# Kernel tuning notes

Hardware: AMD Instinct MI355X
Metric: run time of the kernel (lower is better)

The kernel has to match this reference:

```python
import jax, jax.numpy as jnp
import numpy as np

B, L, D_MODEL = 2, 2048, 1024
D_STATE, D_CONV, EXPAND = 8, 4, 2
D_INNER = EXPAND * D_MODEL          # 2048
DT_RANK = (D_MODEL + 15) // 16      # 64


def setup_inputs() -> dict:
    key = jax.random.key(0)
    ks = jax.random.split(key, 8)
    s = 0.02
    x = jax.random.normal(ks[0], (B, L, D_MODEL), dtype=jnp.float32)
    W_in = jax.random.normal(ks[1], (D_MODEL, 2 * D_INNER), dtype=jnp.float32) * s
    dw_kernel = jax.random.normal(ks[2], (D_CONV, D_INNER), dtype=jnp.float32) * s  # depthwise
    pw_kernel = jax.random.normal(ks[3], (D_INNER, D_INNER), dtype=jnp.float32) * s  # pointwise
    conv_bias = jnp.zeros((D_INNER,), dtype=jnp.float32)
    W_x = jax.random.normal(ks[4], (D_INNER, DT_RANK + 2 * D_STATE), dtype=jnp.float32) * s
    W_dt = jax.random.normal(ks[5], (DT_RANK, D_INNER), dtype=jnp.float32) * s
    b_dt = jnp.zeros((D_INNER,), dtype=jnp.float32)
    # A = repeat(range(1..d_state), d_inner).reshape(d_inner, d_state), stored as log
    A_init = np.repeat(np.arange(1, D_STATE + 1, dtype=np.float32), D_INNER).reshape(D_INNER, D_STATE)
    A_log = jnp.asarray(np.log(A_init))
    D = jnp.ones((D_INNER,), dtype=jnp.float32)
    W_out = jax.random.normal(ks[6], (D_INNER, D_MODEL), dtype=jnp.float32) * s
    return {"x": x, "W_in": W_in, "dw_kernel": dw_kernel, "pw_kernel": pw_kernel,
            "conv_bias": conv_bias, "W_x": W_x, "W_dt": W_dt, "b_dt": b_dt,
            "A_log": A_log, "D": D, "W_out": W_out}


def reference(x, W_in, dw_kernel, pw_kernel, conv_bias, W_x, W_dt, b_dt, A_log, D, W_out):
    d_inner, d_state = A_log.shape
    dt_rank = W_dt.shape[0]
    d_conv = dw_kernel.shape[0]
    bsz = x.shape[0]

    xz = x @ W_in                                   # [B,L,2*di]
    x_in, z = jnp.split(xz, 2, axis=-1)             # each [B,L,di]

    # causal separable conv: depthwise (causal pad) -> pointwise -> swish
    xp = jnp.pad(x_in, ((0, 0), (d_conv - 1, 0), (0, 0)))
    xc = jax.lax.conv_general_dilated(
        xp, dw_kernel[:, None, :], window_strides=(1,), padding='VALID',
        dimension_numbers=('NWC', 'WIO', 'NWC'), feature_group_count=d_inner)
    xc = jax.nn.silu(xc @ pw_kernel + conv_bias)    # [B,L,di]

    x_dbl = xc @ W_x                                # [B,L,dt_rank+2*ds]
    delta = x_dbl[..., :dt_rank]
    Bm = x_dbl[..., dt_rank:dt_rank + d_state]      # [B,L,ds]
    C = x_dbl[..., dt_rank + d_state:]              # [B,L,ds]
    delta = jax.nn.softplus(delta @ W_dt + b_dt)    # [B,L,di]

    A = -jnp.exp(A_log)                             # [di,ds]
    deltaA = jnp.exp(jnp.einsum('bld,dn->bldn', delta, A))       # [B,L,di,ds]
    deltaB_u = jnp.einsum('bld,bln,bld->bldn', delta, Bm, xc)    # [B,L,di,ds]

    def step(h, inp):
        dA_t, dBu_t, C_t = inp
        h = dA_t * h + dBu_t                        # [B,di,ds]
        y_t = jnp.einsum('bn,bdn->bd', C_t, h)      # [B,di]
        return h, y_t

    h0 = jnp.zeros((bsz, d_inner, d_state), dtype=x.dtype)
    elems = (deltaA.transpose(1, 0, 2, 3), deltaB_u.transpose(1, 0, 2, 3), C.transpose(1, 0, 2))
    _, ys = jax.lax.scan(step, h0, elems)           # ys: [L,B,di]
    y = ys.transpose(1, 0, 2)                       # [B,L,di]

    y = y + xc * D
    y = y * jax.nn.silu(z)
    return y @ W_out                                # [B,L,d_model]
```

## Files before the change

kernel.cpp:

```cpp
#include <hip/hip_runtime.h>
#include <math.h>

#define Bb 2
#define Ll 2048
#define DMODEL 1024
#define DINNER 2048
#define DSTATE 8
#define DTRANK 64
#define DCONV 4
#define MM (Bb*Ll)
#define NCH 64
#define CL 32
#define G3_KCH 8
#define G3_KC (DINNER / G3_KCH)

typedef __attribute__((ext_vector_type(8))) short    bf16x8;
typedef __attribute__((ext_vector_type(4))) float    f32x4;

__device__ __forceinline__ float silu_f(float x) {
    return x / (1.0f + __expf(-x));
}
__device__ __forceinline__ float softplus_f(float x) {
    return fmaxf(x, 0.0f) + log1pf(__expf(-fabsf(x)));
}
__device__ __forceinline__ unsigned short f2bf(float f) {
    unsigned int u = __float_as_uint(f);
    u += 0x7fffu + ((u >> 16) & 1u);
    return (unsigned short)(u >> 16);
}
__device__ __forceinline__ void async_cp16(const unsigned short* g, unsigned short* l) {
    __builtin_amdgcn_global_load_lds(
        (const __attribute__((address_space(1))) void*)g,
        (__attribute__((address_space(3))) void*)l, 16, 0, 0);
}

template <int EPI>
__global__ __launch_bounds__(256) void mfma_gemm(
    const unsigned short* __restrict__ A, const unsigned short* __restrict__ Bt,
    float* __restrict__ C, int M, int N, int K,
    int lda, int ldb, int ldc, const float* __restrict__ bias)
{
    __shared__ unsigned short As[128 * 32];
    __shared__ unsigned short Bs[128 * 32];

    const int bm = blockIdx.y * 128;
    const int bn = blockIdx.x * 128;
    const int tid  = threadIdx.x;
    const int w    = tid >> 6;
    const int lane = tid & 63;
    const int wm = (w >> 1) * 64;
    const int wn = (w & 1) * 64;
    const int lr = lane & 15;
    const int lq = lane >> 4;

    const int r1 = w * 32 + (lane >> 2);
    const int sp = lane & 3;
    const int slog = sp ^ ((r1 >> 1) & 3);
    const unsigned short* gA1 = A  + (size_t)(bm + r1) * lda + slog * 8;
    const unsigned short* gA2 = gA1 + (size_t)16 * lda;
    const unsigned short* gB1 = Bt + (size_t)(bn + r1) * ldb + slog * 8;
    const unsigned short* gB2 = gB1 + (size_t)16 * ldb;
    unsigned short* lA1 = As + w * 1024;
    unsigned short* lA2 = As + w * 1024 + 512;
    unsigned short* lB1 = Bs + w * 1024;
    unsigned short* lB2 = Bs + w * 1024 + 512;

    const int fsw = (lq ^ ((lr >> 1) & 3)) * 8;

    f32x4 acc[4][4];
#pragma unroll
    for (int i = 0; i < 4; ++i)
#pragma unroll
        for (int j = 0; j < 4; ++j) acc[i][j] = (f32x4){0.f, 0.f, 0.f, 0.f};

    for (int k0 = 0; k0 < K; k0 += 32) {
        __syncthreads();
        async_cp16(gA1 + k0, lA1);
        async_cp16(gA2 + k0, lA2);
        async_cp16(gB1 + k0, lB1);
        async_cp16(gB2 + k0, lB2);
        __syncthreads();

        bf16x8 a[4], b[4];
#pragma unroll
        for (int i = 0; i < 4; ++i)
            a[i] = *(const bf16x8*)&As[(wm + i * 16 + lr) * 32 + fsw];
#pragma unroll
        for (int j = 0; j < 4; ++j)
            b[j] = *(const bf16x8*)&Bs[(wn + j * 16 + lr) * 32 + fsw];
#pragma unroll
        for (int i = 0; i < 4; ++i)
#pragma unroll
            for (int j = 0; j < 4; ++j)
                acc[i][j] = __builtin_amdgcn_mfma_f32_16x16x32_bf16(
                    a[i], b[j], acc[i][j], 0, 0, 0);
    }

#pragma unroll
    for (int i = 0; i < 4; ++i) {
        const int row0 = bm + wm + i * 16 + lq * 4;
#pragma unroll
        for (int j = 0; j < 4; ++j) {
            const int col = bn + wn + j * 16 + lr;
            float bv = (EPI == 1) ? bias[col] : 0.0f;
#pragma unroll
            for (int r = 0; r < 4; ++r) {
                float v = acc[i][j][r];
                if (EPI == 1) v = silu_f(v + bv);
                C[(size_t)(row0 + r) * ldc + col] = v;
            }
        }
    }
}

__global__ __launch_bounds__(256) void gemm_tiled_sp(
    const float* __restrict__ A, const float* __restrict__ B,
    float* __restrict__ C, int M, int N, int K,
    int lda, int ldb, int ldc, const float* __restrict__ bias)
{
    __shared__ float As[16][68];
    __shared__ float Bs[16][68];

    const int bm = blockIdx.y * 64;
    const int bn = blockIdx.x * 64;
    const int tid = threadIdx.x;
    const int tx = tid & 15;
    const int ty = tid >> 4;

    float acc[4][4];
#pragma unroll
    for (int i = 0; i < 4; ++i)
#pragma unroll
        for (int j = 0; j < 4; ++j) acc[i][j] = 0.0f;

    const int ar = tid >> 2;
    const int ac = (tid & 3) << 2;
    const int br = tid >> 4;
    const int bc = (tid & 15) << 2;

    for (int k0 = 0; k0 < K; k0 += 16) {
        float4 av = *(const float4*)&A[(size_t)(bm + ar) * lda + k0 + ac];
        float4 bv = *(const float4*)&B[(size_t)(k0 + br) * ldb + bn + bc];
        As[ac + 0][ar] = av.x;
        As[ac + 1][ar] = av.y;
        As[ac + 2][ar] = av.z;
        As[ac + 3][ar] = av.w;
        *(float4*)&Bs[br][bc] = bv;
        __syncthreads();
#pragma unroll
        for (int k = 0; k < 16; ++k) {
            float4 a4 = *(float4*)&As[k][ty * 4];
            float4 b4 = *(float4*)&Bs[k][tx * 4];
            float am[4] = {a4.x, a4.y, a4.z, a4.w};
            float bn4[4] = {b4.x, b4.y, b4.z, b4.w};
#pragma unroll
            for (int i = 0; i < 4; ++i)
#pragma unroll
                for (int j = 0; j < 4; ++j)
                    acc[i][j] = fmaf(am[i], bn4[j], acc[i][j]);
        }
        __syncthreads();
    }

    const int col = bn + tx * 4;
#pragma unroll
    for (int i = 0; i < 4; ++i) {
        int row = bm + ty * 4 + i;
        float4 v = make_float4(acc[i][0], acc[i][1], acc[i][2], acc[i][3]);
        v.x = softplus_f(v.x + bias[col + 0]);
        v.y = softplus_f(v.y + bias[col + 1]);
        v.z = softplus_f(v.z + bias[col + 2]);
        v.w = softplus_f(v.w + bias[col + 3]);
        *(float4*)&C[(size_t)row * ldc + col] = v;
    }
}

__global__ __launch_bounds__(256) void g3_splitk(
    const float* __restrict__ xc, const float* __restrict__ Wx,
    float* __restrict__ part)
{
    __shared__ float As[16][68];
    __shared__ float Bs[16][85];
    const int m0 = blockIdx.x * 64;
    const int kb = blockIdx.y * G3_KC;
    const int t = threadIdx.x;
    const int tr = t >> 4;
    const int tc = t & 15;

    const int arow = t >> 2;
    const int ak4  = (t & 3) * 4;
    const int bk   = t >> 4;
    const int bc   = (t & 15) * 5;

    float acc[4][5];
#pragma unroll
    for (int r = 0; r < 4; ++r)
#pragma unroll
        for (int c = 0; c < 5; ++c) acc[r][c] = 0.0f;

    for (int k0 = 0; k0 < G3_KC; k0 += 16) {
        float4 av = *(const float4*)&xc[(size_t)(m0 + arow) * DINNER + kb + k0 + ak4];
        float bv[5];
#pragma unroll
        for (int q = 0; q < 5; ++q)
            bv[q] = Wx[(size_t)(kb + k0 + bk) * 80 + bc + q];
        __syncthreads();
        As[ak4 + 0][arow] = av.x;
        As[ak4 + 1][arow] = av.y;
        As[ak4 + 2][arow] = av.z;
        As[ak4 + 3][arow] = av.w;
#pragma unroll
        for (int q = 0; q < 5; ++q) Bs[bk][bc + q] = bv[q];
        __syncthreads();
#pragma unroll
        for (int k = 0; k < 16; ++k) {
            float a[4], b[5];
#pragma unroll
            for (int r = 0; r < 4; ++r) a[r] = As[k][tr * 4 + r];
#pragma unroll
            for (int c = 0; c < 5; ++c) b[c] = Bs[k][tc * 5 + c];
#pragma unroll
            for (int r = 0; r < 4; ++r)
#pragma unroll
                for (int c = 0; c < 5; ++c)
                    acc[r][c] = fmaf(a[r], b[c], acc[r][c]);
        }
    }
#pragma unroll
    for (int r = 0; r < 4; ++r)
#pragma unroll
        for (int c = 0; c < 5; ++c)
            part[((size_t)blockIdx.y * MM + m0 + tr * 4 + r) * 80 + tc * 5 + c] = acc[r][c];
}

__global__ __launch_bounds__(256) void g3_reduce(
    const float* __restrict__ part, float* __restrict__ xdbl)
{
    int i = (blockIdx.x * 256 + threadIdx.x) * 4;
    if (i >= MM * 80) return;
    float4 s = *(const float4*)&part[i];
#pragma unroll
    for (int c = 1; c < G3_KCH; ++c) {
        float4 p = *(const float4*)&part[(size_t)c * MM * 80 + i];
        s.x += p.x; s.y += p.y; s.z += p.z; s.w += p.w;
    }
    *(float4*)&xdbl[i] = s;
}

__global__ __launch_bounds__(256) void transpose_cast(
    const float* __restrict__ src, unsigned short* __restrict__ dst, int R, int C)
{
    __shared__ float tile[32][33];
    const int c0 = blockIdx.x * 32;
    const int r0 = blockIdx.y * 32;
    const int tx = threadIdx.x;
    const int ty = threadIdx.y;
#pragma unroll
    for (int i = 0; i < 32; i += 8)
        tile[ty + i][tx] = src[(size_t)(r0 + ty + i) * C + c0 + tx];
    __syncthreads();
#pragma unroll
    for (int i = 0; i < 32; i += 8)
        dst[(size_t)(c0 + ty + i) * R + r0 + tx] = f2bf(tile[tx][ty + i]);
}

__global__ __launch_bounds__(256) void cast_bf16(
    const float* __restrict__ src, unsigned short* __restrict__ dst, int n)
{
    int i = (blockIdx.x * 256 + threadIdx.x) * 4;
    if (i >= n) return;
    float4 v = *(const float4*)&src[i];
    ushort4 o;
    o.x = f2bf(v.x); o.y = f2bf(v.y); o.z = f2bf(v.z); o.w = f2bf(v.w);
    *(ushort4*)&dst[i] = o;
}

__global__ __launch_bounds__(256) void dwconv_kernel(
    const float* __restrict__ x_in, const float* __restrict__ dwk,
    unsigned short* __restrict__ out)
{
    size_t i = (size_t)blockIdx.x * 256 + threadIdx.x;
    if (i >= (size_t)MM * DINNER) return;
    int d = (int)(i & (DINNER - 1));
    size_t bl = i >> 11;
    int l = (int)(bl & (Ll - 1));
    int b = (int)(bl >> 11);
    float acc = 0.0f;
#pragma unroll
    for (int k = 0; k < DCONV; ++k) {
        int t = l + k - (DCONV - 1);
        if (t >= 0)
            acc = fmaf(x_in[((size_t)(b * Ll + t)) * DINNER + d],
                       dwk[k * DINNER + d], acc);
    }
    out[i] = f2bf(acc);
}

__global__ __launch_bounds__(256) void scan_pass1(
    const float* __restrict__ delta, const float* __restrict__ xc,
    const float* __restrict__ xdbl, const float* __restrict__ A_log,
    float* __restrict__ cs_a, float* __restrict__ cs_h)
{
    const int d = blockIdx.x * 256 + threadIdx.x;
    const int c = blockIdx.y;
    const int b = blockIdx.z;
    const int t0 = c * CL;

    __shared__ float sB[CL][8];
    {
        int i = threadIdx.x;
        int t = i >> 3, j = i & 7;
        sB[t][j] = xdbl[((size_t)(b * Ll + t0 + t)) * 80 + DTRANK + j];
    }
    __syncthreads();

    float An[8];
#pragma unroll
    for (int n = 0; n < 8; ++n) An[n] = -__expf(A_log[d * 8 + n]);

    float h[8], ap[8];
#pragma unroll
    for (int n = 0; n < 8; ++n) { h[n] = 0.0f; ap[n] = 1.0f; }

    const float* dptr = delta + ((size_t)(b * Ll + t0)) * DINNER + d;
    const float* xptr = xc + ((size_t)(b * Ll + t0)) * DINNER + d;

#pragma unroll 4
    for (int t = 0; t < CL; ++t) {
        float dl = dptr[(size_t)t * DINNER];
        float xv = xptr[(size_t)t * DINNER];
        float du = dl * xv;
#pragma unroll
        for (int n = 0; n < 8; ++n) {
            float dA = __expf(dl * An[n]);
            h[n] = fmaf(dA, h[n], du * sB[t][n]);
            ap[n] *= dA;
        }
    }

    size_t base = (((size_t)(b * NCH + c)) * 8) * DINNER + d;
#pragma unroll
    for (int n = 0; n < 8; ++n) {
        cs_a[base + (size_t)n * DINNER] = ap[n];
        cs_h[base + (size_t)n * DINNER] = h[n];
    }
}

__global__ __launch_bounds__(256) void scan_pass2(
    const float* __restrict__ cs_a, const float* cs_h, float* hin)
{
    int idx = blockIdx.x * 256 + threadIdx.x;
    if (idx >= Bb * 8 * DINNER) return;
    int d = idx & (DINNER - 1);
    int n = (idx >> 11) & 7;
    int b = idx >> 14;
    float H = 0.0f;
    for (int c = 0; c < NCH; ++c) {
        size_t o = (((size_t)(b * NCH + c)) * 8 + n) * DINNER + d;
        float a = cs_a[o];
        float hh = cs_h[o];
        hin[o] = H;
        H = fmaf(a, H, hh);
    }
}

__global__ __launch_bounds__(256) void scan_pass3(
    const float* __restrict__ delta, const float* __restrict__ xc,
    const float* __restrict__ xdbl, const float* __restrict__ A_log,
    const float* __restrict__ hin, const float* __restrict__ z,
    const float* __restrict__ Dvec, unsigned short* __restrict__ y_bf)
{
    const int d = blockIdx.x * 256 + threadIdx.x;
    const int c = blockIdx.y;
    const int b = blockIdx.z;
    const int t0 = c * CL;

    __shared__ float sB[CL][8];
    __shared__ float sC[CL][8];
    {
        int i = threadIdx.x;
        int t = i >> 4, j = i & 15;
        float v = xdbl[((size_t)(b * Ll + t0 + t)) * 80 + DTRANK + j];
        if (j < 8) sB[t][j] = v; else sC[t][j - 8] = v;
        t = (i + 256) >> 4; j = (i + 256) & 15;
        v = xdbl[((size_t)(b * Ll + t0 + t)) * 80 + DTRANK + j];
        if (j < 8) sB[t][j] = v; else sC[t][j - 8] = v;
    }
    __syncthreads();

    float An[8];
#pragma unroll
    for (int n = 0; n < 8; ++n) An[n] = -__expf(A_log[d * 8 + n]);

    float h[8];
    size_t hbase = (((size_t)(b * NCH + c)) * 8) * DINNER + d;
#pragma unroll
    for (int n = 0; n < 8; ++n) h[n] = hin[hbase + (size_t)n * DINNER];

    const float Dd = Dvec[d];
    const float* dptr = delta + ((size_t)(b * Ll + t0)) * DINNER + d;
    const float* xptr = xc + ((size_t)(b * Ll + t0)) * DINNER + d;
    const float* zptr = z + ((size_t)(b * Ll + t0)) * DINNER + d;
    unsigned short* yptr = y_bf + ((size_t)(b * Ll + t0)) * DINNER + d;

    for (int t = 0; t < CL; ++t) {
        float dl = dptr[(size_t)t * DINNER];
        float xv = xptr[(size_t)t * DINNER];
        float du = dl * xv;
        float yt = 0.0f;
#pragma unroll
        for (int n = 0; n < 8; ++n) {
            float dA = __expf(dl * An[n]);
            h[n] = fmaf(dA, h[n], du * sB[t][n]);
            yt = fmaf(sC[t][n], h[n], yt);
        }
        float zv = zptr[(size_t)t * DINNER];
        yptr[(size_t)t * DINNER] = f2bf((yt + xv * Dd) * silu_f(zv));
    }
}

extern "C" void kernel_launch(void* const* d_in, const int* in_sizes, int n_in,
                              void* d_out, int out_size, void* d_ws, size_t ws_size,
                              hipStream_t stream)
{
    const float* x         = (const float*)d_in[0];
    const float* W_in      = (const float*)d_in[1];
    const float* dwk       = (const float*)d_in[2];
    const float* pwk       = (const float*)d_in[3];
    const float* conv_bias = (const float*)d_in[4];
    const float* W_x       = (const float*)d_in[5];
    const float* W_dt      = (const float*)d_in[6];
    const float* b_dt      = (const float*)d_in[7];
    const float* A_log     = (const float*)d_in[8];
    const float* Dv        = (const float*)d_in[9];
    const float* W_out     = (const float*)d_in[10];
    float* out = (float*)d_out;

    char* ws = (char*)d_ws;
    float*          x_in   = (float*)(ws);
    float*          delta  = (float*)(ws);
    float*          z      = (float*)(ws + (32ull  << 20));
    unsigned short* x_bf   = (unsigned short*)(ws + (64ull << 20));
    unsigned short* Wint   = (unsigned short*)(ws + (72ull << 20));
    unsigned short* y_bf   = (unsigned short*)(ws + (64ull << 20));
    unsigned short* pw_t   = (unsigned short*)(ws + (80ull << 20));
    unsigned short* Woutt  = (unsigned short*)(ws + (80ull << 20));
    float*          xc     = (float*)(ws + (88ull  << 20));
    unsigned short* xcp_bf = (unsigned short*)(ws + (120ull << 20));
    float*          cs_a   = (float*)(ws + (120ull << 20));
    float*          cs_h   = (float*)(ws + (128ull << 20));
    float*          xdbl   = (float*)(ws + (136ull << 20));
    float*          g3part = (float*)(ws + (138ull << 20));
    float*          hin    = cs_h;

    dim3 blk(256);

    cast_bf16<<<(MM * DMODEL / 4 + 255) / 256, blk, 0, stream>>>(x, x_bf, MM * DMODEL);
    transpose_cast<<<dim3((2 * DINNER) / 32, DMODEL / 32), dim3(32, 8), 0, stream>>>(
        W_in, Wint, DMODEL, 2 * DINNER);
    transpose_cast<<<dim3(DINNER / 32, DINNER / 32), dim3(32, 8), 0, stream>>>(
        pwk, pw_t, DINNER, DINNER);

    mfma_gemm<0><<<dim3(DINNER / 128, MM / 128), blk, 0, stream>>>(
        x_bf, Wint, x_in, MM, DINNER, DMODEL, DMODEL, DMODEL, DINNER, nullptr);
    mfma_gemm<0><<<dim3(DINNER / 128, MM / 128), blk, 0, stream>>>(
        x_bf, Wint + (size_t)DINNER * DMODEL, z, MM, DINNER, DMODEL,
        DMODEL, DMODEL, DINNER, nullptr);

    dwconv_kernel<<<(MM * DINNER + 255) / 256, blk, 0, stream>>>(x_in, dwk, xcp_bf);

    mfma_gemm<1><<<dim3(DINNER / 128, MM / 128), blk, 0, stream>>>(
        xcp_bf, pw_t, xc, MM, DINNER, DINNER, DINNER, DINNER, DINNER, conv_bias);

    transpose_cast<<<dim3(DMODEL / 32, DINNER / 32), dim3(32, 8), 0, stream>>>(
        W_out, Woutt, DINNER, DMODEL);

    g3_splitk<<<dim3(MM / 64, G3_KCH), blk, 0, stream>>>(xc, W_x, g3part);
    g3_reduce<<<(MM * 80 / 4 + 255) / 256, blk, 0, stream>>>(g3part, xdbl);

    gemm_tiled_sp<<<dim3(DINNER / 64, MM / 64), blk, 0, stream>>>(
        xdbl, W_dt, delta, MM, DINNER, DTRANK, 80, DINNER, DINNER, b_dt);

    scan_pass1<<<dim3(DINNER / 256, NCH, Bb), blk, 0, stream>>>(
        delta, xc, xdbl, A_log, cs_a, cs_h);
    scan_pass2<<<(Bb * 8 * DINNER + 255) / 256, blk, 0, stream>>>(cs_a, cs_h, hin);
    scan_pass3<<<dim3(DINNER / 256, NCH, Bb), blk, 0, stream>>>(
        delta, xc, xdbl, A_log, hin, z, Dv, y_bf);

    mfma_gemm<0><<<dim3(DMODEL / 128, MM / 128), blk, 0, stream>>>(
        y_bf, Woutt, out, MM, DMODEL, DINNER, DINNER, DINNER, DMODEL, nullptr);
}
```

Baseline: 439.1 us.

## Double-buffer MFMA GEMM, merge in-projection GEMMs, store xc as bf16

```diff
diff --git a/kernel.cpp b/kernel.cpp
--- a/kernel.cpp
+++ b/kernel.cpp
@@ -28,20 +28,23 @@
     u += 0x7fffu + ((u >> 16) & 1u);
     return (unsigned short)(u >> 16);
 }
+__device__ __forceinline__ float bf2f(unsigned short u) {
+    return __uint_as_float(((unsigned int)u) << 16);
+}
 __device__ __forceinline__ void async_cp16(const unsigned short* g, unsigned short* l) {
     __builtin_amdgcn_global_load_lds(
         (const __attribute__((address_space(1))) void*)g,
         (__attribute__((address_space(3))) void*)l, 16, 0, 0);
 }
 
-template <int EPI>
+template <int EPI, typename OT>
 __global__ __launch_bounds__(256) void mfma_gemm(
     const unsigned short* __restrict__ A, const unsigned short* __restrict__ Bt,
-    float* __restrict__ C, int M, int N, int K,
+    OT* __restrict__ C, int M, int N, int K,
     int lda, int ldb, int ldc, const float* __restrict__ bias)
 {
-    __shared__ unsigned short As[128 * 32];
-    __shared__ unsigned short Bs[128 * 32];
+    __shared__ unsigned short As[2][128 * 32];
+    __shared__ unsigned short Bs[2][128 * 32];
 
     const int bm = blockIdx.y * 128;
     const int bn = blockIdx.x * 128;
@@ -60,10 +63,8 @@
     const unsigned short* gA2 = gA1 + (size_t)16 * lda;
     const unsigned short* gB1 = Bt + (size_t)(bn + r1) * ldb + slog * 8;
     const unsigned short* gB2 = gB1 + (size_t)16 * ldb;
-    unsigned short* lA1 = As + w * 1024;
-    unsigned short* lA2 = As + w * 1024 + 512;
-    unsigned short* lB1 = Bs + w * 1024;
-    unsigned short* lB2 = Bs + w * 1024 + 512;
+    const int st1 = w * 1024;
+    const int st2 = w * 1024 + 512;
 
     const int fsw = (lq ^ ((lr >> 1) & 3)) * 8;
 
@@ -73,21 +74,30 @@
 #pragma unroll
         for (int j = 0; j < 4; ++j) acc[i][j] = (f32x4){0.f, 0.f, 0.f, 0.f};
 
-    for (int k0 = 0; k0 < K; k0 += 32) {
+    async_cp16(gA1, &As[0][st1]);
+    async_cp16(gA2, &As[0][st2]);
+    async_cp16(gB1, &Bs[0][st1]);
+    async_cp16(gB2, &Bs[0][st2]);
+
+    int cur = 0;
+    for (int k0 = 0; k0 < K; k0 += 32, cur ^= 1) {
         __syncthreads();
-        async_cp16(gA1 + k0, lA1);
-        async_cp16(gA2 + k0, lA2);
-        async_cp16(gB1 + k0, lB1);
-        async_cp16(gB2 + k0, lB2);
-        __syncthreads();
+        const int nk = k0 + 32;
+        if (nk < K) {
+            const int nb = cur ^ 1;
+            async_cp16(gA1 + nk, &As[nb][st1]);
+            async_cp16(gA2 + nk, &As[nb][st2]);
+            async_cp16(gB1 + nk, &Bs[nb][st1]);
+            async_cp16(gB2 + nk, &Bs[nb][st2]);
+        }
 
         bf16x8 a[4], b[4];
 #pragma unroll
         for (int i = 0; i < 4; ++i)
-            a[i] = *(const bf16x8*)&As[(wm + i * 16 + lr) * 32 + fsw];
+            a[i] = *(const bf16x8*)&As[cur][(wm + i * 16 + lr) * 32 + fsw];
 #pragma unroll
         for (int j = 0; j < 4; ++j)
-            b[j] = *(const bf16x8*)&Bs[(wn + j * 16 + lr) * 32 + fsw];
+            b[j] = *(const bf16x8*)&Bs[cur][(wn + j * 16 + lr) * 32 + fsw];
 #pragma unroll
         for (int i = 0; i < 4; ++i)
 #pragma unroll
@@ -107,7 +117,10 @@
             for (int r = 0; r < 4; ++r) {
                 float v = acc[i][j][r];
                 if (EPI == 1) v = silu_f(v + bv);
-                C[(size_t)(row0 + r) * ldc + col] = v;
+                if (sizeof(OT) == 2)
+                    C[(size_t)(row0 + r) * ldc + col] = (OT)f2bf(v);
+                else
+                    C[(size_t)(row0 + r) * ldc + col] = (OT)v;
             }
         }
     }
@@ -176,7 +189,7 @@
 }
 
 __global__ __launch_bounds__(256) void g3_splitk(
-    const float* __restrict__ xc, const float* __restrict__ Wx,
+    const unsigned short* __restrict__ xc, const float* __restrict__ Wx,
     float* __restrict__ part)
 {
     __shared__ float As[16][68];
@@ -199,16 +212,16 @@
         for (int c = 0; c < 5; ++c) acc[r][c] = 0.0f;
 
     for (int k0 = 0; k0 < G3_KC; k0 += 16) {
-        float4 av = *(const float4*)&xc[(size_t)(m0 + arow) * DINNER + kb + k0 + ak4];
+        ushort4 av = *(const ushort4*)&xc[(size_t)(m0 + arow) * DINNER + kb + k0 + ak4];
         float bv[5];
 #pragma unroll
         for (int q = 0; q < 5; ++q)
             bv[q] = Wx[(size_t)(kb + k0 + bk) * 80 + bc + q];
         __syncthreads();
-        As[ak4 + 0][arow] = av.x;
-        As[ak4 + 1][arow] = av.y;
-        As[ak4 + 2][arow] = av.z;
-        As[ak4 + 3][arow] = av.w;
+        As[ak4 + 0][arow] = bf2f(av.x);
+        As[ak4 + 1][arow] = bf2f(av.y);
+        As[ak4 + 2][arow] = bf2f(av.z);
+        As[ak4 + 3][arow] = bf2f(av.w);
 #pragma unroll
         for (int q = 0; q < 5; ++q) Bs[bk][bc + q] = bv[q];
         __syncthreads();
@@ -276,7 +289,7 @@
 }
 
 __global__ __launch_bounds__(256) void dwconv_kernel(
-    const float* __restrict__ x_in, const float* __restrict__ dwk,
+    const float* __restrict__ xz, const float* __restrict__ dwk,
     unsigned short* __restrict__ out)
 {
     size_t i = (size_t)blockIdx.x * 256 + threadIdx.x;
@@ -290,14 +303,14 @@
     for (int k = 0; k < DCONV; ++k) {
         int t = l + k - (DCONV - 1);
         if (t >= 0)
-            acc = fmaf(x_in[((size_t)(b * Ll + t)) * DINNER + d],
+            acc = fmaf(xz[((size_t)(b * Ll + t)) * (2 * DINNER) + d],
                        dwk[k * DINNER + d], acc);
     }
     out[i] = f2bf(acc);
 }
 
 __global__ __launch_bounds__(256) void scan_pass1(
-    const float* __restrict__ delta, const float* __restrict__ xc,
+    const float* __restrict__ delta, const unsigned short* __restrict__ xc,
     const float* __restrict__ xdbl, const float* __restrict__ A_log,
     float* __restrict__ cs_a, float* __restrict__ cs_h)
 {
@@ -323,12 +336,12 @@
     for (int n = 0; n < 8; ++n) { h[n] = 0.0f; ap[n] = 1.0f; }
 
     const float* dptr = delta + ((size_t)(b * Ll + t0)) * DINNER + d;
-    const float* xptr = xc + ((size_t)(b * Ll + t0)) * DINNER + d;
+    const unsigned short* xptr = xc + ((size_t)(b * Ll + t0)) * DINNER + d;
 
 #pragma unroll 4
     for (int t = 0; t < CL; ++t) {
         float dl = dptr[(size_t)t * DINNER];
-        float xv = xptr[(size_t)t * DINNER];
+        float xv = bf2f(xptr[(size_t)t * DINNER]);
         float du = dl * xv;
 #pragma unroll
         for (int n = 0; n < 8; ++n) {
@@ -365,9 +378,9 @@
 }
 
 __global__ __launch_bounds__(256) void scan_pass3(
-    const float* __restrict__ delta, const float* __restrict__ xc,
+    const float* __restrict__ delta, const unsigned short* __restrict__ xc,
     const float* __restrict__ xdbl, const float* __restrict__ A_log,
-    const float* __restrict__ hin, const float* __restrict__ z,
+    const float* __restrict__ hin, const float* __restrict__ xz,
     const float* __restrict__ Dvec, unsigned short* __restrict__ y_bf)
 {
     const int d = blockIdx.x * 256 + threadIdx.x;
@@ -399,13 +412,13 @@
 
     const float Dd = Dvec[d];
     const float* dptr = delta + ((size_t)(b * Ll + t0)) * DINNER + d;
-    const float* xptr = xc + ((size_t)(b * Ll + t0)) * DINNER + d;
-    const float* zptr = z + ((size_t)(b * Ll + t0)) * DINNER + d;
+    const unsigned short* xptr = xc + ((size_t)(b * Ll + t0)) * DINNER + d;
+    const float* zptr = xz + ((size_t)(b * Ll + t0)) * (2 * DINNER) + DINNER + d;
     unsigned short* yptr = y_bf + ((size_t)(b * Ll + t0)) * DINNER + d;
 
     for (int t = 0; t < CL; ++t) {
         float dl = dptr[(size_t)t * DINNER];
-        float xv = xptr[(size_t)t * DINNER];
+        float xv = bf2f(xptr[(size_t)t * DINNER]);
         float du = dl * xv;
         float yt = 0.0f;
 #pragma unroll
@@ -414,7 +427,7 @@
             h[n] = fmaf(dA, h[n], du * sB[t][n]);
             yt = fmaf(sC[t][n], h[n], yt);
         }
-        float zv = zptr[(size_t)t * DINNER];
+        float zv = zptr[(size_t)t * (2 * DINNER)];
         yptr[(size_t)t * DINNER] = f2bf((yt + xv * Dd) * silu_f(zv));
     }
 }
@@ -437,20 +450,19 @@
     float* out = (float*)d_out;
 
     char* ws = (char*)d_ws;
-    float*          x_in   = (float*)(ws);
-    float*          delta  = (float*)(ws);
-    float*          z      = (float*)(ws + (32ull  << 20));
-    unsigned short* x_bf   = (unsigned short*)(ws + (64ull << 20));
-    unsigned short* Wint   = (unsigned short*)(ws + (72ull << 20));
-    unsigned short* y_bf   = (unsigned short*)(ws + (64ull << 20));
-    unsigned short* pw_t   = (unsigned short*)(ws + (80ull << 20));
-    unsigned short* Woutt  = (unsigned short*)(ws + (80ull << 20));
-    float*          xc     = (float*)(ws + (88ull  << 20));
-    unsigned short* xcp_bf = (unsigned short*)(ws + (120ull << 20));
-    float*          cs_a   = (float*)(ws + (120ull << 20));
-    float*          cs_h   = (float*)(ws + (128ull << 20));
-    float*          xdbl   = (float*)(ws + (136ull << 20));
-    float*          g3part = (float*)(ws + (138ull << 20));
+    float*          xz     = (float*)(ws);
+    unsigned short* x_bf   = (unsigned short*)(ws + (64ull  << 20));
+    unsigned short* Wint   = (unsigned short*)(ws + (72ull  << 20));
+    float*          g3part = (float*)(ws + (64ull  << 20));
+    float*          delta  = (float*)(ws + (64ull  << 20));
+    unsigned short* pw_t   = (unsigned short*)(ws + (96ull  << 20));
+    float*          cs_a   = (float*)(ws + (96ull  << 20));
+    unsigned short* xcp_bf = (unsigned short*)(ws + (104ull << 20));
+    float*          cs_h   = (float*)(ws + (104ull << 20));
+    unsigned short* Woutt  = (unsigned short*)(ws + (112ull << 20));
+    float*          xdbl   = (float*)(ws + (116ull << 20));
+    unsigned short* xc_bf  = (unsigned short*)(ws + (120ull << 20));
+    unsigned short* y_bf   = (unsigned short*)(ws + (136ull << 20));
     float*          hin    = cs_h;
 
     dim3 blk(256);
@@ -461,32 +473,29 @@
     transpose_cast<<<dim3(DINNER / 32, DINNER / 32), dim3(32, 8), 0, stream>>>(
         pwk, pw_t, DINNER, DINNER);
 
-    mfma_gemm<0><<<dim3(DINNER / 128, MM / 128), blk, 0, stream>>>(
-        x_bf, Wint, x_in, MM, DINNER, DMODEL, DMODEL, DMODEL, DINNER, nullptr);
-    mfma_gemm<0><<<dim3(DINNER / 128, MM / 128), blk, 0, stream>>>(
-        x_bf, Wint + (size_t)DINNER * DMODEL, z, MM, DINNER, DMODEL,
-        DMODEL, DMODEL, DINNER, nullptr);
-
-    dwconv_kernel<<<(MM * DINNER + 255) / 256, blk, 0, stream>>>(x_in, dwk, xcp_bf);
-
-    mfma_gemm<1><<<dim3(DINNER / 128, MM / 128), blk, 0, stream>>>(
-        xcp_bf, pw_t, xc, MM, DINNER, DINNER, DINNER, DINNER, DINNER, conv_bias);
+    mfma_gemm<0, float><<<dim3((2 * DINNER) / 128, MM / 128), blk, 0, stream>>>(
+        x_bf, Wint, xz, MM, 2 * DINNER, DMODEL, DMODEL, DMODEL, 2 * DINNER, nullptr);
+
+    dwconv_kernel<<<(MM * DINNER + 255) / 256, blk, 0, stream>>>(xz, dwk, xcp_bf);
+
+    mfma_gemm<1, unsigned short><<<dim3(DINNER / 128, MM / 128), blk, 0, stream>>>(
+        xcp_bf, pw_t, xc_bf, MM, DINNER, DINNER, DINNER, DINNER, DINNER, conv_bias);
 
     transpose_cast<<<dim3(DMODEL / 32, DINNER / 32), dim3(32, 8), 0, stream>>>(
         W_out, Woutt, DINNER, DMODEL);
 
-    g3_splitk<<<dim3(MM / 64, G3_KCH), blk, 0, stream>>>(xc, W_x, g3part);
+    g3_splitk<<<dim3(MM / 64, G3_KCH), blk, 0, stream>>>(xc_bf, W_x, g3part);
     g3_reduce<<<(MM * 80 / 4 + 255) / 256, blk, 0, stream>>>(g3part, xdbl);
 
     gemm_tiled_sp<<<dim3(DINNER / 64, MM / 64), blk, 0, stream>>>(
         xdbl, W_dt, delta, MM, DINNER, DTRANK, 80, DINNER, DINNER, b_dt);
 
     scan_pass1<<<dim3(DINNER / 256, NCH, Bb), blk, 0, stream>>>(
-        delta, xc, xdbl, A_log, cs_a, cs_h);
+        delta, xc_bf, xdbl, A_log, cs_a, cs_h);
     scan_pass2<<<(Bb * 8 * DINNER + 255) / 256, blk, 0, stream>>>(cs_a, cs_h, hin);
     scan_pass3<<<dim3(DINNER / 256, NCH, Bb), blk, 0, stream>>>(
-        delta, xc, xdbl, A_log, hin, z, Dv, y_bf);
-
-    mfma_gemm<0><<<dim3(DMODEL / 128, MM / 128), blk, 0, stream>>>(
+        delta, xc_bf, xdbl, A_log, hin, xz, Dv, y_bf);
+
+    mfma_gemm<0, float><<<dim3(DMODEL / 128, MM / 128), blk, 0, stream>>>(
         y_bf, Woutt, out, MM, DMODEL, DINNER, DINNER, DINNER, DMODEL, nullptr);
 }
```

Result: faster. 419.1 us (-4.5%).
